# Optimization experiments

Measured on AMD Instinct MI355X. Metric: run time of the kernel, lower is better.

## Reference

```python
import jax, jax.numpy as jnp
import numpy as np

GRID_SIZE = 5
SPLINE_ORDER = 3
GRID_RANGE = (-1.0, 1.0)
LAYERS = [1024, 1024, 1024]
BATCH = 8192
LN_EPS = 1e-5


def _make_grid(in_features):
    h = (GRID_RANGE[1] - GRID_RANGE[0]) / GRID_SIZE
    n = GRID_SIZE + 2 * SPLINE_ORDER + 1  # 12 knots
    g = jnp.linspace(GRID_RANGE[0] - h * SPLINE_ORDER,
                     GRID_RANGE[1] + h * SPLINE_ORDER, n, dtype=jnp.float32)
    return jnp.broadcast_to(g, (in_features, n))


def setup_inputs() -> dict:
    key = jax.random.key(0)
    ks = jax.random.split(key, 8)
    n_layers = len(LAYERS) - 1
    d_in, d_out = LAYERS[0], LAYERS[1]  # square layers -> stackable params
    coeff = GRID_SIZE + SPLINE_ORDER  # 8
    # kaiming_uniform_(nonlinearity='linear'): bound = sqrt(3) * (1/sqrt(fan_in))
    bw_bound = float(np.sqrt(3.0) / np.sqrt(d_in))
    sw_bound = float(np.sqrt(3.0) / np.sqrt(d_in * coeff))
    x = jax.random.normal(ks[0], (BATCH, d_in), dtype=jnp.float32)
    base_w = jax.random.uniform(ks[1], (n_layers, d_out, d_in), jnp.float32, -bw_bound, bw_bound)
    spline_w = jax.random.uniform(ks[2], (n_layers, d_out, d_in, coeff), jnp.float32, -sw_bound, sw_bound)
    ln_g = jnp.ones((n_layers, d_out), jnp.float32)
    ln_b = jnp.zeros((n_layers, d_out), jnp.float32)
    prelu_a = jnp.full((n_layers,), 0.25, jnp.float32)
    grid = jnp.stack([_make_grid(d_in) for _ in range(n_layers)])  # [L, in, 12]
    return {"x": x, "base_w": base_w, "spline_w": spline_w,
            "ln_g": ln_g, "ln_b": ln_b, "prelu_a": prelu_a, "grid": grid}


def _bspline_bases(x, g):
    """Cox-de Boor recursion. x: [B, in], g: [in, n_knots] -> [B, in, G+order]."""
    xu = x[..., None]  # [B, in, 1]
    bases = ((xu >= g[:, :-1]) & (xu < g[:, 1:])).astype(x.dtype)  # [B, in, 11]
    for k in range(1, SPLINE_ORDER + 1):
        left = g[:, :-(k + 1)]
        right = g[:, k:-1]
        delta = jnp.where(right == left, jnp.ones_like(right), right - left)
        bases = ((xu - left) / delta * bases[..., :-1]
                 + (g[:, k + 1:] - xu) / (g[:, k + 1:] - g[:, 1:-k]) * bases[..., 1:])
    return bases  # [B, in, 8]


def kan_forward(x, base_w, spline_w, ln_g, ln_b, prelu_a, grid):
    n_layers = base_w.shape[0]
    for i in range(n_layers):
        base_out = jnp.matmul(jax.nn.gelu(x, approximate=False), base_w[i].T)  # [B, out]
        bases = _bspline_bases(x, grid[i])  # [B, in, 8]
        spline_out = jnp.matmul(bases.reshape(x.shape[0], -1),
                                spline_w[i].reshape(spline_w.shape[1], -1).T)  # [B, out]
        h = base_out + spline_out
        mu = jnp.mean(h, axis=-1, keepdims=True)
        var = jnp.var(h, axis=-1, keepdims=True)  # biased, matches torch LayerNorm
        h = (h - mu) * jax.lax.rsqrt(var + LN_EPS) * ln_g[i] + ln_b[i]
        x = jnp.where(h >= 0, h, prelu_a[i] * h)  # PReLU (scalar slope per layer)
    return x


def reference(x, base_w, spline_w, ln_g, ln_b, prelu_a, grid):
    return kan_forward(x, base_w, spline_w, ln_g, ln_b, prelu_a, grid)
```

## Files before the change

kernel.cpp:

```cpp
#include <hip/hip_runtime.h>
#include <hip/hip_bf16.h>
#include <cstdint>
#include <cstddef>

typedef __bf16 bf16_t;
typedef __bf16 bf16x8 __attribute__((ext_vector_type(8)));
typedef __bf16 bf16x4 __attribute__((ext_vector_type(4)));
typedef float  f32x4  __attribute__((ext_vector_type(4)));

#define DIM    1024
#define NCOEF  8
#define KTOT   (DIM + DIM * NCOEF)
#define NKNOT  12
#define BATCH  8192
#define LN_EPS 1e-5f

__device__ __forceinline__ float gelu_exact(float x) {
    return 0.5f * x * (1.0f + erff(x * 0.70710678118654752440f));
}

__device__ __forceinline__ void gl_lds16(const void* g, void* l) {
    __builtin_amdgcn_global_load_lds(
        (const __attribute__((address_space(1))) unsigned int*)(uintptr_t)g,
        (__attribute__((address_space(3))) unsigned int*)(uintptr_t)l, 16, 0, 0);
}

__device__ __forceinline__ uint64_t pack4bf(float a, float b, float c, float d) {
    union { bf16_t h[4]; uint64_t q; } u;
    u.h[0] = (bf16_t)a; u.h[1] = (bf16_t)b; u.h[2] = (bf16_t)c; u.h[3] = (bf16_t)d;
    return u.q;
}

__device__ __forceinline__ void spline8(float x, float g0, float invh,
                                        uint64_t& lo, uint64_t& hi) {
    float u = (x - g0) * invh;
    float jf = floorf(u);
    int j = (int)jf;
    float f = u - jf;
    float f2 = f * f, f3 = f2 * f;
    float om = 1.0f - f, om2 = om * om;
    float w0 = om2 * om * (1.0f / 6.0f);
    float w3 = f3 * (1.0f / 6.0f);
    float w1 = fmaf(0.5f, f3, 2.0f / 3.0f) - f2;
    float w2 = 1.0f - w0 - w1 - w3;
    uint64_t W64 = pack4bf(w0, w1, w2, w3);
    if (!(u >= 0.0f && u < 11.0f)) W64 = 0;
    int sh = (j - 3) * 16;
    if (sh >= 0) {
        int s = sh & 63;
        uint64_t loW = W64 << s;
        uint64_t hiW = s ? (W64 >> (64 - s)) : 0ull;
        lo = (sh < 64) ? loW : 0ull;
        hi = (sh < 64) ? hiW : loW;
    } else {
        lo = W64 >> (-sh);
        hi = 0ull;
    }
}

__global__ void pack_w(const float* __restrict__ bw, const float* __restrict__ sw,
                       bf16_t* __restrict__ W) {
    int idx = blockIdx.x * 256 + threadIdx.x;
    bf16_t* wrow = W + (size_t)(idx >> 10) * KTOT;
    int j = idx & 1023;
    wrow[j] = (bf16_t)bw[idx];
    const float4* sp = (const float4*)(sw + (size_t)idx * NCOEF);
    float4 s0 = sp[0], s1 = sp[1];
    bf16x8 v;
    v[0] = (bf16_t)s0.x; v[1] = (bf16_t)s0.y; v[2] = (bf16_t)s0.z; v[3] = (bf16_t)s0.w;
    v[4] = (bf16_t)s1.x; v[5] = (bf16_t)s1.y; v[6] = (bf16_t)s1.z; v[7] = (bf16_t)s1.w;
    *(bf16x8*)(wrow + DIM + j * NCOEF) = v;
}

__global__ void prep_A(const float* __restrict__ x, bf16_t* __restrict__ A,
                       const float* __restrict__ gp, int R) {
    const int t = threadIdx.x;
    const float g0 = gp[0];
    const float invh = 1.0f / (gp[1] - gp[0]);
    for (int row = blockIdx.x; row < R; row += gridDim.x) {
        f32x4 v = *(const f32x4*)(x + (size_t)row * DIM + t * 4);
        bf16_t* Ar = A + (size_t)row * KTOT;
        bf16x4 ge;
#pragma unroll
        for (int k = 0; k < 4; k++) ge[k] = (bf16_t)gelu_exact(v[k]);
        *(bf16x4*)(Ar + t * 4) = ge;
#pragma unroll
        for (int k = 0; k < 4; k++) {
            uint64_t lo, hi;
            union { uint64_t u[2]; uint4 q; } o;
            spline8(v[k], g0, invh, lo, hi);
            o.u[0] = lo; o.u[1] = hi;
            *(uint4*)(Ar + DIM + (t * 4 + k) * NCOEF) = o.q;
        }
    }
}


#define STR2(x) #x
#define GATEV(N) asm volatile("s_waitcnt vmcnt(" STR2(N) ")" ::: "memory");
#define LGKM0    asm volatile("s_waitcnt lgkmcnt(0)" ::: "memory");
#define BAR() { __builtin_amdgcn_s_barrier(); asm volatile("" ::: "memory"); }

#define RD_A(DST, BO, G) { \
    const bf16_t* p_ = ldsA + (BO) + aOffBase + (G) * 2048; \
    DST[0][0] = *(const bf16x8*)(p_);        DST[1][0] = *(const bf16x8*)(p_ + 512); \
    DST[2][0] = *(const bf16x8*)(p_ + 1024); DST[3][0] = *(const bf16x8*)(p_ + 1536); \
    DST[0][1] = *(const bf16x8*)(p_ + 4096); DST[1][1] = *(const bf16x8*)(p_ + 4608); \
    DST[2][1] = *(const bf16x8*)(p_ + 5120); DST[3][1] = *(const bf16x8*)(p_ + 5632); }

#define RD_B(DST, BO, CG) { \
    const bf16_t* p_ = ldsB + (BO) + bOffBase + (CG) * 1024; \
    DST[0][0] = *(const bf16x8*)(p_);        DST[1][0] = *(const bf16x8*)(p_ + 512); \
    DST[0][1] = *(const bf16x8*)(p_ + 4096); DST[1][1] = *(const bf16x8*)(p_ + 4608); }

#define STG_A(TILE, HALF) { \
    const bf16_t* s_ = AgS + (size_t)(HALF) * (128 * (size_t)KTOT) + (size_t)(TILE) * 64; \
    bf16_t* d_ = ldsA + (((TILE) & 1) * 16384) + (HALF) * 8192 + tid * 8; \
    gl_lds16(s_, d_); gl_lds16(s_ + 32, d_ + 4096); }

#define STG_B(TILE, HALF) { \
    const bf16_t* s_ = BgS + (size_t)(HALF) * (128 * (size_t)KTOT) + (size_t)(TILE) * 64; \
    bf16_t* d_ = ldsB + (((TILE) & 1) * 16384) + (HALF) * 8192 + tid * 8; \
    gl_lds16(s_, d_); gl_lds16(s_ + 32, d_ + 4096); }

#define MFQ(G, CG, AS, BS) { \
    _Pragma("unroll") \
    for (int ks_ = 0; ks_ < 2; ks_++) \
    _Pragma("unroll") \
    for (int fr_ = 0; fr_ < 4; fr_++) \
    _Pragma("unroll") \
    for (int cf_ = 0; cf_ < 2; cf_++) \
        acc[(G) * 4 + fr_][(CG) * 2 + cf_] = __builtin_amdgcn_mfma_f32_16x16x32_bf16( \
            AS[fr_][ks_], BS[cf_][ks_], acc[(G) * 4 + fr_][(CG) * 2 + cf_], 0, 0, 0); }

#define PHX(MF, ENDG) \
    BAR() LGKM0 __builtin_amdgcn_sched_barrier(0); \
    __builtin_amdgcn_s_setprio(1); MF __builtin_amdgcn_s_setprio(0); \
    ENDG BAR()

#define ITER8(T, S12, S34, S56, S78, G4T, G8T) { \
     \
    RD_A(Ar0, 0, 0) RD_B(Bc0, 0, 0) \
    if (S12) { STG_B((T) + 1, 0) } \
    PHX(MFQ(0, 0, Ar0, Bc0), ;) \
     \
    RD_A(Ar1, 0, 1) \
    if (S12) { STG_B((T) + 1, 1) } \
    PHX(MFQ(1, 0, Ar1, Bc0), ;) \
     \
    RD_B(Bc1, 0, 1) \
    if (S34) { STG_A((T) + 2, 0) } \
    PHX(MFQ(1, 1, Ar1, Bc1), ;) \
     \
    if (S34) { STG_A((T) + 2, 1) } \
    PHX(MFQ(0, 1, Ar0, Bc1), G4T) \
     \
    RD_A(Ar0, 16384, 0) RD_B(Bc0, 16384, 0) \
    if (S56) { STG_B((T) + 2, 0) } \
    PHX(MFQ(0, 0, Ar0, Bc0), ;) \
     \
    RD_A(Ar1, 16384, 1) \
    if (S56) { STG_B((T) + 2, 1) } \
    PHX(MFQ(1, 0, Ar1, Bc0), ;) \
     \
    RD_B(Bc1, 16384, 1) \
    if (S78) { STG_A((T) + 3, 0) } \
    PHX(MFQ(1, 1, Ar1, Bc1), ;) \
     \
    if (S78) { STG_A((T) + 3, 1) } \
    PHX(MFQ(0, 1, Ar0, Bc1), G8T) \
}

template<int NTK>
__global__ __launch_bounds__(512, 2) void gemm_ab(
    const bf16_t* __restrict__ A,
    const bf16_t* __restrict__ W,
    float* __restrict__ C,
    int mmask, int mshift, int rows) {
    __shared__ __align__(16) bf16_t lds[65536];
    bf16_t* __restrict__ ldsA = lds;
    bf16_t* __restrict__ ldsB = lds + 32768;

    const int tid = threadIdx.x;
    const int l = tid & 63, wv = tid >> 6;
    const int wm = wv >> 2, wn = wv & 3;

    const int chunk = gridDim.x >> 3;
    const int bid = blockIdx.x;
    const int wg = (bid & 7) * chunk + (bid >> 3);
    const int bm = wg & mmask;
    const int bn = (wg >> mshift) & 3;
    const int ks = wg >> (mshift + 2);
    const int row0 = bm << 8, col0 = bn << 8;
    const int koff0 = ks * (NTK * 64);

    const int srow = tid >> 2;
    const int schunk = (tid & 3) ^ ((srow >> 1) & 3);
    const bf16_t* __restrict__ AgS = A + (size_t)(row0 + srow) * KTOT + koff0 + schunk * 8;
    const bf16_t* __restrict__ BgS = W + (size_t)(col0 + srow) * KTOT + koff0 + schunk * 8;

    const int l15 = l & 15;
    const int pc = (l >> 4) ^ ((l15 >> 1) & 3);
    const int aOffBase = wm * 8192 + l15 * 32 + pc * 8;
    const int bOffBase = (wn >> 1) * 8192 + (wn & 1) * 2048 + l15 * 32 + pc * 8;

    f32x4 acc[8][4] = {};
    bf16x8 Ar0[4][2], Ar1[4][2], Bc0[2][2], Bc1[2][2];

    STG_A(0, 0) STG_A(0, 1)
    STG_B(0, 0) STG_B(0, 1)
    STG_A(1, 0) STG_A(1, 1)
    GATEV(4)
    BAR()

#pragma unroll 1
    for (int i = 0; i < NTK / 2 - 1; i++) {
        const int T = 2 * i;
        ITER8(T, 1, 1, 1, 1, GATEV(4), GATEV(4))
    }
    ITER8(NTK - 2, 1, 0, 0, 0, GATEV(0), ;)

    float* __restrict__ Cp = C + (size_t)ks * rows * DIM;
    const int r0 = row0 + wm * 128 + (l >> 4) * 4;
    const int c0 = col0 + wn * 64 + l15;
#pragma unroll
    for (int i = 0; i < 8; i++)
#pragma unroll
        for (int j = 0; j < 4; j++)
#pragma unroll
            for (int r = 0; r < 4; r++)
                Cp[(size_t)(r0 + i * 16 + r) * DIM + c0 + j * 16] = acc[i][j][r];
}

__global__ void ln_mid_A(const float* __restrict__ h, int rows, int ksplit,
                         const float* __restrict__ g_ln, const float* __restrict__ b_ln,
                         const float* __restrict__ pa, bf16_t* __restrict__ A,
                         const float* __restrict__ gp) {
    const int tid = threadIdx.x;
    const int w = tid >> 6, l = tid & 63;
    const float a = pa[0];
    const float g0 = gp[0];
    const float invh = 1.0f / (gp[1] - gp[0]);
    __shared__ float rs[4], rq[4];
    for (int row = blockIdx.x; row < rows; row += gridDim.x) {
        f32x4 v = {0.0f, 0.0f, 0.0f, 0.0f};
        for (int ks = 0; ks < ksplit; ks++)
            v += *(const f32x4*)(h + ((size_t)ks * rows + row) * DIM + tid * 4);
        float s = v[0] + v[1] + v[2] + v[3];
        float q = v[0] * v[0] + v[1] * v[1] + v[2] * v[2] + v[3] * v[3];
#pragma unroll
        for (int o = 32; o > 0; o >>= 1) { s += __shfl_xor(s, o); q += __shfl_xor(q, o); }
        if (l == 0) { rs[w] = s; rq[w] = q; }
        __syncthreads();
        s = rs[0] + rs[1] + rs[2] + rs[3];
        q = rq[0] + rq[1] + rq[2] + rq[3];
        __syncthreads();
        float mean = s * (1.0f / DIM);
        float var = q * (1.0f / DIM) - mean * mean;
        float rstd = rsqrtf(var + LN_EPS);
        bf16_t* Ar = A + (size_t)row * KTOT;
        bf16x4 ge;
#pragma unroll
        for (int c = 0; c < 4; c++) {
            int col = tid * 4 + c;
            float yv = (v[c] - mean) * rstd * g_ln[col] + b_ln[col];
            yv = (yv >= 0.0f) ? yv : a * yv;
            ge[c] = (bf16_t)gelu_exact(yv);
            uint64_t lo, hi;
            union { uint64_t u[2]; uint4 qv; } o;
            spline8(yv, g0, invh, lo, hi);
            o.u[0] = lo; o.u[1] = hi;
            *(uint4*)(Ar + DIM + (size_t)col * NCOEF) = o.qv;
        }
        *(bf16x4*)(Ar + tid * 4) = ge;
    }
}

__global__ void ln_out(const float* __restrict__ h, int rows, int ksplit,
                       const float* __restrict__ g_ln, const float* __restrict__ b_ln,
                       const float* __restrict__ pa, float* __restrict__ out) {
    const int tid = threadIdx.x;
    const int w = tid >> 6, l = tid & 63;
    const float a = pa[0];
    __shared__ float rs[4], rq[4];
    for (int row = blockIdx.x; row < rows; row += gridDim.x) {
        f32x4 v = {0.0f, 0.0f, 0.0f, 0.0f};
        for (int ks = 0; ks < ksplit; ks++)
            v += *(const f32x4*)(h + ((size_t)ks * rows + row) * DIM + tid * 4);
        float s = v[0] + v[1] + v[2] + v[3];
        float q = v[0] * v[0] + v[1] * v[1] + v[2] * v[2] + v[3] * v[3];
#pragma unroll
        for (int o = 32; o > 0; o >>= 1) { s += __shfl_xor(s, o); q += __shfl_xor(q, o); }
        if (l == 0) { rs[w] = s; rq[w] = q; }
        __syncthreads();
        s = rs[0] + rs[1] + rs[2] + rs[3];
        q = rq[0] + rq[1] + rq[2] + rq[3];
        __syncthreads();
        float mean = s * (1.0f / DIM);
        float var = q * (1.0f / DIM) - mean * mean;
        float rstd = rsqrtf(var + LN_EPS);
        f32x4 o4;
#pragma unroll
        for (int c = 0; c < 4; c++) {
            int col = tid * 4 + c;
            float yv = (v[c] - mean) * rstd * g_ln[col] + b_ln[col];
            o4[c] = (yv >= 0.0f) ? yv : a * yv;
        }
        *(f32x4*)(out + (size_t)row * DIM + tid * 4) = o4;
    }
}

extern "C" void kernel_launch(void* const* d_in, const int* in_sizes, int n_in,
                              void* d_out, int out_size, void* d_ws, size_t ws_size,
                              hipStream_t stream) {
    const float* x    = (const float*)d_in[0];
    const float* bw   = (const float*)d_in[1];
    const float* sw   = (const float*)d_in[2];
    const float* ln_g = (const float*)d_in[3];
    const float* ln_b = (const float*)d_in[4];
    const float* pa   = (const float*)d_in[5];
    const float* gridK = (const float*)d_in[6];
    float* out = (float*)d_out;

    const size_t wbytes = (size_t)2 * DIM * KTOT * sizeof(bf16_t);
    int R = 8192, ksplit = 2;
    for (;;) {
        size_t need = wbytes + (size_t)R * KTOT * 2 + (size_t)ksplit * R * DIM * 4;
        if (need <= ws_size || R == 512) break;
        R >>= 1;
        int mt = R / 256;
        ksplit = (mt >= 32) ? 2 : (mt >= 16) ? 4 : 8;
    }
    int mtiles = R / 256;
    int mshift = 0; while ((1 << mshift) < mtiles) mshift++;
    int mmask = mtiles - 1;
    int grid = mtiles * 4 * ksplit;
    int lng = (R >= 2048) ? 2048 : R;

    char* wsc = (char*)d_ws;
    bf16_t* Wbuf = (bf16_t*)wsc;
    bf16_t* Abuf = (bf16_t*)(wsc + wbytes);
    float*  hbuf = (float*)(wsc + wbytes + (size_t)R * KTOT * 2);

    pack_w<<<(2 * DIM * DIM) / 256, 256, 0, stream>>>(bw, sw, Wbuf);

    auto launch_gemm = [&](const bf16_t* Wl, hipStream_t st) {
        if (ksplit == 2)
            gemm_ab<72><<<grid, 512, 0, st>>>(Abuf, Wl, hbuf, mmask, mshift, R);
        else if (ksplit == 4)
            gemm_ab<36><<<grid, 512, 0, st>>>(Abuf, Wl, hbuf, mmask, mshift, R);
        else
            gemm_ab<18><<<grid, 512, 0, st>>>(Abuf, Wl, hbuf, mmask, mshift, R);
    };

    const int nslab = BATCH / R;
    for (int sidx = 0; sidx < nslab; sidx++) {
        const size_t row0 = (size_t)sidx * R;
        const float* x0 = x + row0 * DIM;
        prep_A<<<lng, 256, 0, stream>>>(x0, Abuf, gridK, R);
        launch_gemm(Wbuf, stream);
        ln_mid_A<<<lng, 256, 0, stream>>>(hbuf, R, ksplit, ln_g, ln_b, pa,
                                          Abuf, gridK + DIM * NKNOT);
        launch_gemm(Wbuf + (size_t)DIM * KTOT, stream);
        ln_out<<<lng, 256, 0, stream>>>(hbuf, R, ksplit, ln_g + DIM, ln_b + DIM,
                                        pa + 1, out + row0 * DIM);
    }
}
```

Baseline: 512.2 us.

## Reschedule GEMM main loop phases to overlap LDS reads with MFMA

After: 533.9 us. +4.2%, slower.

```diff
diff --git a/kernel.cpp b/kernel.cpp
--- a/kernel.cpp
+++ b/kernel.cpp
@@ -98,14 +98,20 @@
 
 #define STR2(x) #x
 #define GATEV(N) asm volatile("s_waitcnt vmcnt(" STR2(N) ")" ::: "memory");
-#define LGKM0    asm volatile("s_waitcnt lgkmcnt(0)" ::: "memory");
+#define LGKM(N)  asm volatile("s_waitcnt lgkmcnt(" STR2(N) ")" ::: "memory");
 #define BAR() { __builtin_amdgcn_s_barrier(); asm volatile("" ::: "memory"); }
-
-#define RD_A(DST, BO, G) { \
+#define SCH0 __builtin_amdgcn_sched_barrier(0);
+#define SP1 __builtin_amdgcn_s_setprio(1);
+#define SP0 __builtin_amdgcn_s_setprio(0);
+
+#define RD_A_LO(DST, BO, G) { \
     const bf16_t* p_ = ldsA + (BO) + aOffBase + (G) * 2048; \
     DST[0][0] = *(const bf16x8*)(p_);        DST[1][0] = *(const bf16x8*)(p_ + 512); \
+    DST[0][1] = *(const bf16x8*)(p_ + 4096); DST[1][1] = *(const bf16x8*)(p_ + 4608); }
+
+#define RD_A_HI(DST, BO, G) { \
+    const bf16_t* p_ = ldsA + (BO) + aOffBase + (G) * 2048; \
     DST[2][0] = *(const bf16x8*)(p_ + 1024); DST[3][0] = *(const bf16x8*)(p_ + 1536); \
-    DST[0][1] = *(const bf16x8*)(p_ + 4096); DST[1][1] = *(const bf16x8*)(p_ + 4608); \
     DST[2][1] = *(const bf16x8*)(p_ + 5120); DST[3][1] = *(const bf16x8*)(p_ + 5632); }
 
 #define RD_B(DST, BO, CG) { \
@@ -123,52 +129,58 @@
     bf16_t* d_ = ldsB + (((TILE) & 1) * 16384) + (HALF) * 8192 + tid * 8; \
     gl_lds16(s_, d_); gl_lds16(s_ + 32, d_ + 4096); }
 
-#define MFQ(G, CG, AS, BS) { \
+#define MFQ_HALF(G, CG, AS, BS, F0) { \
+    _Pragma("unroll") \
+    for (int fr_ = (F0); fr_ < (F0) + 2; fr_++) \
     _Pragma("unroll") \
     for (int ks_ = 0; ks_ < 2; ks_++) \
-    _Pragma("unroll") \
-    for (int fr_ = 0; fr_ < 4; fr_++) \
     _Pragma("unroll") \
     for (int cf_ = 0; cf_ < 2; cf_++) \
         acc[(G) * 4 + fr_][(CG) * 2 + cf_] = __builtin_amdgcn_mfma_f32_16x16x32_bf16( \
             AS[fr_][ks_], BS[cf_][ks_], acc[(G) * 4 + fr_][(CG) * 2 + cf_], 0, 0, 0); }
 
-#define PHX(MF, ENDG) \
-    BAR() LGKM0 __builtin_amdgcn_sched_barrier(0); \
-    __builtin_amdgcn_s_setprio(1); MF __builtin_amdgcn_s_setprio(0); \
-    ENDG BAR()
-
-#define ITER8(T, S12, S34, S56, S78, G4T, G8T) { \
-     \
-    RD_A(Ar0, 0, 0) RD_B(Bc0, 0, 0) \
-    if (S12) { STG_B((T) + 1, 0) } \
-    PHX(MFQ(0, 0, Ar0, Bc0), ;) \
-     \
-    RD_A(Ar1, 0, 1) \
-    if (S12) { STG_B((T) + 1, 1) } \
-    PHX(MFQ(1, 0, Ar1, Bc0), ;) \
-     \
-    RD_B(Bc1, 0, 1) \
-    if (S34) { STG_A((T) + 2, 0) } \
-    PHX(MFQ(1, 1, Ar1, Bc1), ;) \
-     \
-    if (S34) { STG_A((T) + 2, 1) } \
-    PHX(MFQ(0, 1, Ar0, Bc1), G4T) \
-     \
-    RD_A(Ar0, 16384, 0) RD_B(Bc0, 16384, 0) \
-    if (S56) { STG_B((T) + 2, 0) } \
-    PHX(MFQ(0, 0, Ar0, Bc0), ;) \
-     \
-    RD_A(Ar1, 16384, 1) \
-    if (S56) { STG_B((T) + 2, 1) } \
-    PHX(MFQ(1, 0, Ar1, Bc0), ;) \
-     \
-    RD_B(Bc1, 16384, 1) \
-    if (S78) { STG_A((T) + 3, 0) } \
-    PHX(MFQ(1, 1, Ar1, Bc1), ;) \
-     \
-    if (S78) { STG_A((T) + 3, 1) } \
-    PHX(MFQ(0, 1, Ar0, Bc1), G8T) \
+#define MFQ_FULL(G, CG, AS, BS) MFQ_HALF(G, CG, AS, BS, 0) MFQ_HALF(G, CG, AS, BS, 2)
+
+#define PH_HEAVY(STGS, BO, RDTAIL) \
+    STGS \
+    BAR() \
+    RD_B(Bc0, BO, 0) \
+    RD_A_LO(Ar0, BO, 0) \
+    SCH0 \
+    RD_A_HI(Ar0, BO, 0) \
+    LGKM(4) SCH0 \
+    SP1 MFQ_HALF(0, 0, Ar0, Bc0, 0) SP0 \
+    LGKM(0) SCH0 \
+    SP1 MFQ_HALF(0, 0, Ar0, Bc0, 2) SP0 \
+    RDTAIL
+
+#define PH_STD(STGS, MF, TAIL) \
+    STGS \
+    BAR() \
+    LGKM(0) SCH0 \
+    SP1 MF SP0 \
+    TAIL
+
+#define ITER8(T, SF, G4S, G8S) { \
+     \
+    PH_HEAVY({ STG_A((T) + 1, 0) STG_A((T) + 1, 1) }, 0, RD_B(Bc1, 0, 1)) \
+     \
+    PH_STD({ STG_B((T) + 1, 1) }, MFQ_FULL(0, 1, Ar0, Bc1), \
+           RD_A_LO(Ar1, 0, 1) RD_A_HI(Ar1, 0, 1)) \
+     \
+    PH_STD(;, MFQ_FULL(1, 1, Ar1, Bc1), ;) \
+     \
+    PH_STD({ if (SF) { STG_B((T) + 2, 0) } }, MFQ_FULL(1, 0, Ar1, Bc0), G4S) \
+     \
+    PH_HEAVY({ if (SF) { STG_A((T) + 2, 0) STG_A((T) + 2, 1) } }, 16384, \
+             RD_B(Bc1, 16384, 1)) \
+     \
+    PH_STD({ if (SF) { STG_B((T) + 2, 1) } }, MFQ_FULL(0, 1, Ar0, Bc1), \
+           RD_A_LO(Ar1, 16384, 1) RD_A_HI(Ar1, 16384, 1)) \
+     \
+    PH_STD(;, MFQ_FULL(1, 1, Ar1, Bc1), ;) \
+     \
+    PH_STD({ if (SF) { STG_B((T) + 3, 0) } }, MFQ_FULL(1, 0, Ar1, Bc0), G8S) \
 }
 
 template<int NTK>
@@ -209,16 +221,16 @@
 
     STG_A(0, 0) STG_A(0, 1)
     STG_B(0, 0) STG_B(0, 1)
-    STG_A(1, 0) STG_A(1, 1)
-    GATEV(4)
+    STG_B(1, 0)
+    GATEV(2)
     BAR()
 
 #pragma unroll 1
     for (int i = 0; i < NTK / 2 - 1; i++) {
         const int T = 2 * i;
-        ITER8(T, 1, 1, 1, 1, GATEV(4), GATEV(4))
-    }
-    ITER8(NTK - 2, 1, 0, 0, 0, GATEV(0), ;)
+        ITER8(T, 1, GATEV(2), GATEV(2))
+    }
+    ITER8(NTK - 2, 0, GATEV(0), ;)
 
     float* __restrict__ Cp = C + (size_t)ks * rows * DIM;
     const int r0 = row0 + wm * 128 + (l >> 4) * 4;
```
